# Performance work log

Measured on AMD Instinct MI355X. Metric: run time of the kernel, lower is better.

Reference implementation:

```python
import jax, jax.numpy as jnp
import numpy as np

N_NODES = 50000
N_EDGES = 800000
D_IN = 128
D_HID = 128
N_CLS = 40


def setup_inputs() -> dict:
    key = jax.random.key(0)
    ks = jax.random.split(key, 8)
    x = jax.random.normal(ks[0], (N_NODES, D_IN), dtype=jnp.float32)
    edge_index = jax.random.randint(ks[1], (2, N_EDGES), 0, N_NODES, dtype=jnp.int32)
    s1 = 1.0 / np.sqrt(D_IN)
    s2 = 1.0 / np.sqrt(D_HID)
    W1 = jax.random.normal(ks[2], (D_IN, D_HID), dtype=jnp.float32) * s1
    b1 = jnp.zeros((D_HID,), dtype=jnp.float32)
    W2 = jax.random.normal(ks[3], (D_HID, D_HID), dtype=jnp.float32) * s2
    b2 = jnp.zeros((D_HID,), dtype=jnp.float32)
    Wc = jax.random.normal(ks[4], (D_HID, N_CLS), dtype=jnp.float32) * s2
    bc = jnp.zeros((N_CLS,), dtype=jnp.float32)
    return {"x": x, "edge_index": edge_index, "W1": W1, "b1": b1,
            "W2": W2, "b2": b2, "Wc": Wc, "bc": bc, "conv_time": 30}


def _gcn_graph(edge_index, n, dtype):
    # add self-loops, compute symmetric GCN normalization D^-1/2 A D^-1/2
    loops = jnp.arange(n, dtype=edge_index.dtype)
    src = jnp.concatenate([edge_index[0], loops])
    dst = jnp.concatenate([edge_index[1], loops])
    deg = jax.ops.segment_sum(jnp.ones_like(src, dtype=dtype), dst, num_segments=n)
    dinv = jnp.where(deg > 0, jax.lax.rsqrt(jnp.maximum(deg, 1.0)), 0.0).astype(dtype)
    w = dinv[src] * dinv[dst]  # [E+N] edge weights
    return src, dst, w


def _propagate_k(h, src, dst, w, n, k):
    # apply normalized aggregation k times (k is a static Python int-compatible value)
    def body(_, hh):
        return jax.ops.segment_sum(hh[src] * w[:, None], dst, num_segments=n)
    return jax.lax.fori_loop(0, k, body, h)


def reference(x, edge_index, W1, b1, W2, b2, Wc, bc, conv_time):
    n = x.shape[0]
    src, dst, w = _gcn_graph(edge_index, n, x.dtype)
    # conv1: linear only (conv_time=0), relu; dropout is identity in eval mode
    h = jax.nn.relu(x @ W1 + b1)
    # conv2: linear + conv_time propagation hops, relu
    h = jax.nn.relu(_propagate_k(h @ W2 + b2, src, dst, w, n, conv_time))
    # cls: linear + 1 propagation hop
    out = _propagate_k(h @ Wc + bc, src, dst, w, n, 1)
    return out
```

## Files before the change

kernel.cpp:

```cpp
#include <hip/hip_runtime.h>
#include <hip/hip_bf16.h>

#define NN 50000
#define NE 800000
#define DH 128
#define NCLS 40
#define HOPS 30

typedef unsigned int uint32;
typedef unsigned short ushort16;


__global__ void count_deg(const int* __restrict__ dst, int* __restrict__ cnt) {
    int e = blockIdx.x * blockDim.x + threadIdx.x;
    if (e < NE) atomicAdd(&cnt[dst[e]], 1);
}

__global__ void calc_dinv(const int* __restrict__ cnt, float* __restrict__ dinv) {
    int v = blockIdx.x * blockDim.x + threadIdx.x;
    if (v < NN) dinv[v] = rsqrtf((float)cnt[v] + 1.0f);
}

__global__ void scan1(const int* __restrict__ cnt, int* __restrict__ rowptr,
                      int* __restrict__ bsum) {
    __shared__ int s[1024];
    int t = threadIdx.x;
    int i = blockIdx.x * 1024 + t;
    int v = (i < NN) ? cnt[i] : 0;
    s[t] = v;
    __syncthreads();
    for (int off = 1; off < 1024; off <<= 1) {
        int add = (t >= off) ? s[t - off] : 0;
        __syncthreads();
        s[t] += add;
        __syncthreads();
    }
    if (i < NN) rowptr[i] = s[t] - v;
    if (t == 1023) bsum[blockIdx.x] = s[1023];
}

__global__ void scan2(int* __restrict__ bsum, int* __restrict__ rowptr, int nb) {
    if (blockIdx.x == 0 && threadIdx.x == 0) {
        int run = 0;
        for (int b = 0; b < nb; ++b) { int v = bsum[b]; bsum[b] = run; run += v; }
        rowptr[NN] = run;
    }
}

__global__ void scan3(int* __restrict__ rowptr, const int* __restrict__ bsum,
                      int* __restrict__ cursor) {
    int i = blockIdx.x * 1024 + threadIdx.x;
    if (i < NN) {
        int r = rowptr[i] + bsum[blockIdx.x];
        rowptr[i] = r;
        cursor[i] = r;
    }
}

__global__ void fill_csr(const int* __restrict__ src, const int* __restrict__ dst,
                         const float* __restrict__ dinv, int* __restrict__ cursor,
                         int2* __restrict__ csr) {
    int e = blockIdx.x * blockDim.x + threadIdx.x;
    if (e < NE) {
        int s = src[e], d = dst[e];
        int p = atomicAdd(&cursor[d], 1);
        float w = dinv[s] * dinv[d];
        csr[p] = make_int2(s, __float_as_int(w));
    }
}


__device__ __forceinline__ void unpack8(uint4 u, float* f) {
    f[0] = __uint_as_float(u.x << 16);
    f[1] = __uint_as_float(u.x & 0xffff0000u);
    f[2] = __uint_as_float(u.y << 16);
    f[3] = __uint_as_float(u.y & 0xffff0000u);
    f[4] = __uint_as_float(u.z << 16);
    f[5] = __uint_as_float(u.z & 0xffff0000u);
    f[6] = __uint_as_float(u.w << 16);
    f[7] = __uint_as_float(u.w & 0xffff0000u);
}

__device__ __forceinline__ ushort16 f2bf(float x) {
    __hip_bfloat16 b = __float2bfloat16(x);
    return *reinterpret_cast<ushort16*>(&b);
}


template <bool RELU, bool BF16OUT>
__global__ __launch_bounds__(256) void gemm128(const float* __restrict__ A,
                                               const float* __restrict__ W,
                                               const float* __restrict__ bias,
                                               void* __restrict__ C, int n) {
    __shared__ float xs[64 * 128];
    __shared__ float ws[32 * 128];
    const int t = threadIdx.x;
    const int row0 = blockIdx.x * 64;

    const float4* A4 = reinterpret_cast<const float4*>(A);
    float4* xs4 = reinterpret_cast<float4*>(xs);
    for (int i = t; i < 64 * 32; i += 256) {
        int r = i >> 5, c4 = i & 31;
        int gr = row0 + r;
        xs4[i] = (gr < n) ? A4[(size_t)gr * 32 + c4] : make_float4(0.f, 0.f, 0.f, 0.f);
    }

    float acc[8][4];
#pragma unroll
    for (int r = 0; r < 8; ++r)
#pragma unroll
        for (int j = 0; j < 4; ++j) acc[r][j] = 0.f;

    const int cb = (t & 31) * 4;
    const int rb = (t >> 5) * 8;
    const float4* W4 = reinterpret_cast<const float4*>(W);
    float4* ws4 = reinterpret_cast<float4*>(ws);

    for (int k0 = 0; k0 < 128; k0 += 32) {
        __syncthreads();
        for (int i = t; i < 32 * 32; i += 256)
            ws4[i] = W4[(size_t)(k0 + (i >> 5)) * 32 + (i & 31)];
        __syncthreads();
#pragma unroll
        for (int kk = 0; kk < 32; ++kk) {
            float4 wv = ws4[kk * 32 + (cb >> 2)];
#pragma unroll
            for (int r = 0; r < 8; ++r) {
                float xv = xs[(rb + r) * 128 + k0 + kk];
                acc[r][0] += xv * wv.x;
                acc[r][1] += xv * wv.y;
                acc[r][2] += xv * wv.z;
                acc[r][3] += xv * wv.w;
            }
        }
    }

    float4 bv = reinterpret_cast<const float4*>(bias)[cb >> 2];
#pragma unroll
    for (int r = 0; r < 8; ++r) {
        int gr = row0 + rb + r;
        if (gr < n) {
            float o[4];
            o[0] = acc[r][0] + bv.x;
            o[1] = acc[r][1] + bv.y;
            o[2] = acc[r][2] + bv.z;
            o[3] = acc[r][3] + bv.w;
            if (RELU) {
#pragma unroll
                for (int j = 0; j < 4; ++j) o[j] = fmaxf(o[j], 0.f);
            }
            if (BF16OUT) {
                ushort16 pk[4];
#pragma unroll
                for (int j = 0; j < 4; ++j) pk[j] = f2bf(o[j]);
                *reinterpret_cast<ushort4*>(reinterpret_cast<ushort16*>(C) +
                                            (size_t)gr * 128 + cb) =
                    *reinterpret_cast<ushort4*>(pk);
            } else {
                float4 ov = make_float4(o[0], o[1], o[2], o[3]);
                reinterpret_cast<float4*>(C)[(size_t)gr * 32 + (cb >> 2)] = ov;
            }
        }
    }
}

__global__ __launch_bounds__(256) void gemm40_bf(const uint4* __restrict__ A,
                                                 const float* __restrict__ W,
                                                 const float* __restrict__ bias,
                                                 float* __restrict__ C, int n) {
    __shared__ float xs[32 * 128];
    __shared__ float wl[128 * 40];
    __shared__ float bl[40];
    const int t = threadIdx.x;
    const int row0 = blockIdx.x * 32;

    for (int i = t; i < 32 * 16; i += 256) {
        int r = i >> 4, c = i & 15, gr = row0 + r;
        uint4 u = (gr < n) ? A[(size_t)gr * 16 + c] : make_uint4(0, 0, 0, 0);
        float f[8];
        unpack8(u, f);
#pragma unroll
        for (int j = 0; j < 8; ++j) xs[r * 128 + c * 8 + j] = f[j];
    }
    for (int i = t; i < 128 * 40; i += 256) wl[i] = W[i];
    if (t < 40) bl[t] = bias[t];
    __syncthreads();

    const int r = t >> 3;
    const int c0 = (t & 7) * 5;
    float acc[5] = {0.f, 0.f, 0.f, 0.f, 0.f};
    for (int k = 0; k < 128; ++k) {
        float xv = xs[r * 128 + k];
#pragma unroll
        for (int j = 0; j < 5; ++j) acc[j] += xv * wl[k * 40 + c0 + j];
    }
    int gr = row0 + r;
    if (gr < n) {
#pragma unroll
        for (int j = 0; j < 5; ++j) C[(size_t)gr * 40 + c0 + j] = acc[j] + bl[c0 + j];
    }
}


__global__ __launch_bounds__(256) void prop_bf(const uint4* __restrict__ hin,
                                               uint4* __restrict__ hout,
                                               const int* __restrict__ rowptr,
                                               const int2* __restrict__ csr,
                                               const float* __restrict__ dinv,
                                               int relu) {
    const int g = threadIdx.x >> 4;
    const int l = threadIdx.x & 15;
    const int v = blockIdx.x * 16 + g;
    if (v >= NN) return;

    const float dv = dinv[v];
    const float wself = dv * dv;

    float acc[8];
    {
        float f[8];
        unpack8(hin[(size_t)v * 16 + l], f);
#pragma unroll
        for (int j = 0; j < 8; ++j) acc[j] = wself * f[j];
    }

    int e = rowptr[v];
    const int end = rowptr[v + 1];
    for (; e + 2 <= end; e += 2) {
        int2 p0 = csr[e];
        int2 p1 = csr[e + 1];
        uint4 a = hin[(size_t)p0.x * 16 + l];
        uint4 b = hin[(size_t)p1.x * 16 + l];
        float w0 = __int_as_float(p0.y);
        float w1 = __int_as_float(p1.y);
        float fa[8], fb[8];
        unpack8(a, fa);
        unpack8(b, fb);
#pragma unroll
        for (int j = 0; j < 8; ++j) acc[j] += w0 * fa[j] + w1 * fb[j];
    }
    if (e < end) {
        int2 p0 = csr[e];
        uint4 a = hin[(size_t)p0.x * 16 + l];
        float w0 = __int_as_float(p0.y);
        float fa[8];
        unpack8(a, fa);
#pragma unroll
        for (int j = 0; j < 8; ++j) acc[j] += w0 * fa[j];
    }

    if (relu) {
#pragma unroll
        for (int j = 0; j < 8; ++j) acc[j] = fmaxf(acc[j], 0.f);
    }

    ushort16 pk[8];
#pragma unroll
    for (int j = 0; j < 8; ++j) pk[j] = f2bf(acc[j]);
    hout[(size_t)v * 16 + l] = *reinterpret_cast<uint4*>(pk);
}

__global__ __launch_bounds__(64) void prop40(const float* __restrict__ z,
                                             float* __restrict__ out,
                                             const int* __restrict__ rowptr,
                                             const int2* __restrict__ csr,
                                             const float* __restrict__ dinv) {
    const int v = blockIdx.x;
    const int d = threadIdx.x;
    if (d >= NCLS) return;
    float dv = dinv[v];
    float acc = dv * dv * z[(size_t)v * NCLS + d];
    const int beg = rowptr[v], end = rowptr[v + 1];
    for (int e = beg; e < end; ++e) {
        int2 p = csr[e];
        acc += __int_as_float(p.y) * z[(size_t)p.x * NCLS + d];
    }
    out[(size_t)v * NCLS + d] = acc;
}


extern "C" void kernel_launch(void* const* d_in, const int* in_sizes, int n_in,
                              void* d_out, int out_size, void* d_ws, size_t ws_size,
                              hipStream_t stream) {
    const float* x   = (const float*)d_in[0];
    const int* edge  = (const int*)d_in[1];
    const float* W1  = (const float*)d_in[2];
    const float* b1  = (const float*)d_in[3];
    const float* W2  = (const float*)d_in[4];
    const float* b2  = (const float*)d_in[5];
    const float* Wc  = (const float*)d_in[6];
    const float* bc  = (const float*)d_in[7];
    const int* esrc = edge;
    const int* edst = edge + NE;
    float* out = (float*)d_out;

    char* w = (char*)d_ws;
    auto alloc = [&](size_t bytes) { void* p = (void*)w; w += (bytes + 255) & ~(size_t)255; return p; };
    int*   cnt    = (int*)  alloc((size_t)NN * 4);
    float* dinv   = (float*)alloc((size_t)NN * 4);
    int*   rowptr = (int*)  alloc((size_t)(NN + 1) * 4);
    int*   bsum   = (int*)  alloc(64 * 4);
    int*   cursor = (int*)  alloc((size_t)NN * 4);
    int2*  csr    = (int2*) alloc((size_t)NE * 8);
    float* h0f    = (float*)alloc((size_t)NN * DH * 4);
    uint4* hb0    = (uint4*)alloc((size_t)NN * DH * 2);
    uint4* hb1    = (uint4*)alloc((size_t)NN * DH * 2);
    float* z      = (float*)alloc((size_t)NN * NCLS * 4);

    const int NB_SCAN = (NN + 1023) / 1024;

    hipMemsetAsync(cnt, 0, (size_t)NN * 4, stream);
    count_deg<<<(NE + 255) / 256, 256, 0, stream>>>(edst, cnt);
    calc_dinv<<<(NN + 255) / 256, 256, 0, stream>>>(cnt, dinv);
    scan1<<<NB_SCAN, 1024, 0, stream>>>(cnt, rowptr, bsum);
    scan2<<<1, 64, 0, stream>>>(bsum, rowptr, NB_SCAN);
    scan3<<<NB_SCAN, 1024, 0, stream>>>(rowptr, bsum, cursor);
    fill_csr<<<(NE + 255) / 256, 256, 0, stream>>>(esrc, edst, dinv, cursor, csr);

    gemm128<true, false><<<(NN + 63) / 64, 256, 0, stream>>>(x, W1, b1, h0f, NN);
    gemm128<false, true><<<(NN + 63) / 64, 256, 0, stream>>>(h0f, W2, b2, hb0, NN);

    uint4* cur = hb0;
    uint4* alt = hb1;
    for (int hop = 0; hop < HOPS; ++hop) {
        prop_bf<<<(NN + 15) / 16, 256, 0, stream>>>(cur, alt, rowptr, csr, dinv,
                                                    (hop == HOPS - 1) ? 1 : 0);
        uint4* tmp = cur; cur = alt; alt = tmp;
    }

    gemm40_bf<<<(NN + 31) / 32, 256, 0, stream>>>(cur, Wc, bc, z, NN);
    prop40<<<NN, 64, 0, stream>>>(z, out, rowptr, csr, dinv);
}
```

Measured before the change: 1.274 ms.

## Use MFMA bf16 GEMMs, feature-sliced propagation, and reorder final propagate before classifier

Replaces the FP32 SIMT GEMMs with bf16 MFMA kernels using pre-transposed bf16 weights. Propagation now splits the 128 features into 8 column slices, one per block, so each hop works on a narrower cache footprint. It also stores only source indices in the CSR and computes edge weights from dinv on the fly. The last hop runs on the 128-wide hidden state before the classifier GEMM (A(hW)=(Ah)W), with the bias scaled by per-node row sums, which removes the narrow prop40 kernel. The input x is now rounded to bf16 before the first GEMM, which reduces precision.

```diff
diff --git a/kernel.cpp b/kernel.cpp
--- a/kernel.cpp
+++ b/kernel.cpp
@@ -9,6 +9,29 @@
 
 typedef unsigned int uint32;
 typedef unsigned short ushort16;
+typedef __attribute__((ext_vector_type(8))) short short8v;
+typedef __attribute__((ext_vector_type(4))) float float4v;
+
+
+__device__ __forceinline__ ushort16 bfbits(float x) {
+    __hip_bfloat16 b = __float2bfloat16(x);
+    return *reinterpret_cast<ushort16*>(&b);
+}
+
+__device__ __forceinline__ void unpack8(uint4 u, float* f) {
+    f[0] = __uint_as_float(u.x << 16);
+    f[1] = __uint_as_float(u.x & 0xffff0000u);
+    f[2] = __uint_as_float(u.y << 16);
+    f[3] = __uint_as_float(u.y & 0xffff0000u);
+    f[4] = __uint_as_float(u.z << 16);
+    f[5] = __uint_as_float(u.z & 0xffff0000u);
+    f[6] = __uint_as_float(u.w << 16);
+    f[7] = __uint_as_float(u.w & 0xffff0000u);
+}
+
+__device__ __forceinline__ uint32 pack2(float a, float b) {
+    return (uint32)bfbits(a) | ((uint32)bfbits(b) << 16);
+}
 
 
 __global__ void count_deg(const int* __restrict__ dst, int* __restrict__ cnt) {
@@ -58,132 +81,207 @@
 }
 
 __global__ void fill_csr(const int* __restrict__ src, const int* __restrict__ dst,
-                         const float* __restrict__ dinv, int* __restrict__ cursor,
-                         int2* __restrict__ csr) {
+                         int* __restrict__ cursor, int* __restrict__ csr_src) {
     int e = blockIdx.x * blockDim.x + threadIdx.x;
     if (e < NE) {
         int s = src[e], d = dst[e];
         int p = atomicAdd(&cursor[d], 1);
-        float w = dinv[s] * dinv[d];
-        csr[p] = make_int2(s, __float_as_int(w));
-    }
-}
-
-
-__device__ __forceinline__ void unpack8(uint4 u, float* f) {
-    f[0] = __uint_as_float(u.x << 16);
-    f[1] = __uint_as_float(u.x & 0xffff0000u);
-    f[2] = __uint_as_float(u.y << 16);
-    f[3] = __uint_as_float(u.y & 0xffff0000u);
-    f[4] = __uint_as_float(u.z << 16);
-    f[5] = __uint_as_float(u.z & 0xffff0000u);
-    f[6] = __uint_as_float(u.w << 16);
-    f[7] = __uint_as_float(u.w & 0xffff0000u);
-}
-
-__device__ __forceinline__ ushort16 f2bf(float x) {
-    __hip_bfloat16 b = __float2bfloat16(x);
-    return *reinterpret_cast<ushort16*>(&b);
-}
-
-
-template <bool RELU, bool BF16OUT>
-__global__ __launch_bounds__(256) void gemm128(const float* __restrict__ A,
-                                               const float* __restrict__ W,
-                                               const float* __restrict__ bias,
-                                               void* __restrict__ C, int n) {
-    __shared__ float xs[64 * 128];
-    __shared__ float ws[32 * 128];
+        csr_src[p] = s;
+    }
+}
+
+
+__global__ void prep_wt(const float* __restrict__ W1, const float* __restrict__ W2,
+                        ushort16* __restrict__ w1t, ushort16* __restrict__ w2t) {
+    int i = blockIdx.x * 256 + threadIdx.x;
+    if (i < 16384) {
+        int n = i >> 7, k = i & 127;
+        w1t[n * 128 + k] = bfbits(W1[k * 128 + n]);
+    } else {
+        int j = i - 16384;
+        int n = j >> 7, k = j & 127;
+        w2t[n * 128 + k] = bfbits(W2[k * 128 + n]);
+    }
+}
+
+
+template <bool AF32, bool RELU>
+__global__ __launch_bounds__(256) void conv_mfma(const void* __restrict__ Ap,
+                                                 const ushort16* __restrict__ WT,
+                                                 const float* __restrict__ bias,
+                                                 ushort16* __restrict__ C) {
     const int t = threadIdx.x;
-    const int row0 = blockIdx.x * 64;
-
-    const float4* A4 = reinterpret_cast<const float4*>(A);
-    float4* xs4 = reinterpret_cast<float4*>(xs);
-    for (int i = t; i < 64 * 32; i += 256) {
-        int r = i >> 5, c4 = i & 31;
-        int gr = row0 + r;
-        xs4[i] = (gr < n) ? A4[(size_t)gr * 32 + c4] : make_float4(0.f, 0.f, 0.f, 0.f);
-    }
-
-    float acc[8][4];
-#pragma unroll
-    for (int r = 0; r < 8; ++r)
-#pragma unroll
-        for (int j = 0; j < 4; ++j) acc[r][j] = 0.f;
-
-    const int cb = (t & 31) * 4;
-    const int rb = (t >> 5) * 8;
-    const float4* W4 = reinterpret_cast<const float4*>(W);
-    float4* ws4 = reinterpret_cast<float4*>(ws);
-
-    for (int k0 = 0; k0 < 128; k0 += 32) {
-        __syncthreads();
-        for (int i = t; i < 32 * 32; i += 256)
-            ws4[i] = W4[(size_t)(k0 + (i >> 5)) * 32 + (i & 31)];
-        __syncthreads();
-#pragma unroll
-        for (int kk = 0; kk < 32; ++kk) {
-            float4 wv = ws4[kk * 32 + (cb >> 2)];
-#pragma unroll
-            for (int r = 0; r < 8; ++r) {
-                float xv = xs[(rb + r) * 128 + k0 + kk];
-                acc[r][0] += xv * wv.x;
-                acc[r][1] += xv * wv.y;
-                acc[r][2] += xv * wv.z;
-                acc[r][3] += xv * wv.w;
+    const int w = t >> 6;
+    const int l = t & 63;
+    const int rb = blockIdx.x * 128 + w * 32;
+    const int lr = l & 15;
+    const int lk = (l >> 4) * 8;
+
+    short8v afr[2][4];
+#pragma unroll
+    for (int rt = 0; rt < 2; ++rt) {
+        int row = rb + rt * 16 + lr;
+        if (row > NN - 1) row = NN - 1;
+#pragma unroll
+        for (int ks = 0; ks < 4; ++ks) {
+            int k0 = ks * 32 + lk;
+            if (AF32) {
+                const float* ap = (const float*)Ap + (size_t)row * 128 + k0;
+                float4 f0 = *(const float4*)ap;
+                float4 f1 = *(const float4*)(ap + 4);
+                short8v s;
+                s[0] = (short)bfbits(f0.x); s[1] = (short)bfbits(f0.y);
+                s[2] = (short)bfbits(f0.z); s[3] = (short)bfbits(f0.w);
+                s[4] = (short)bfbits(f1.x); s[5] = (short)bfbits(f1.y);
+                s[6] = (short)bfbits(f1.z); s[7] = (short)bfbits(f1.w);
+                afr[rt][ks] = s;
+            } else {
+                afr[rt][ks] = *(const short8v*)((const ushort16*)Ap +
+                                                (size_t)row * 128 + k0);
             }
         }
     }
 
-    float4 bv = reinterpret_cast<const float4*>(bias)[cb >> 2];
-#pragma unroll
-    for (int r = 0; r < 8; ++r) {
-        int gr = row0 + rb + r;
-        if (gr < n) {
-            float o[4];
-            o[0] = acc[r][0] + bv.x;
-            o[1] = acc[r][1] + bv.y;
-            o[2] = acc[r][2] + bv.z;
-            o[3] = acc[r][3] + bv.w;
-            if (RELU) {
-#pragma unroll
-                for (int j = 0; j < 4; ++j) o[j] = fmaxf(o[j], 0.f);
-            }
-            if (BF16OUT) {
-                ushort16 pk[4];
-#pragma unroll
-                for (int j = 0; j < 4; ++j) pk[j] = f2bf(o[j]);
-                *reinterpret_cast<ushort4*>(reinterpret_cast<ushort16*>(C) +
-                                            (size_t)gr * 128 + cb) =
-                    *reinterpret_cast<ushort4*>(pk);
-            } else {
-                float4 ov = make_float4(o[0], o[1], o[2], o[3]);
-                reinterpret_cast<float4*>(C)[(size_t)gr * 32 + (cb >> 2)] = ov;
+    float4v acc[2][8];
+#pragma unroll
+    for (int rt = 0; rt < 2; ++rt)
+#pragma unroll
+        for (int ct = 0; ct < 8; ++ct)
+            acc[rt][ct] = (float4v){0.f, 0.f, 0.f, 0.f};
+
+#pragma unroll
+    for (int ks = 0; ks < 4; ++ks) {
+        short8v bfr[8];
+#pragma unroll
+        for (int ct = 0; ct < 8; ++ct)
+            bfr[ct] = *(const short8v*)(WT + (size_t)(ct * 16 + lr) * 128 +
+                                        ks * 32 + lk);
+#pragma unroll
+        for (int ct = 0; ct < 8; ++ct) {
+            acc[0][ct] = __builtin_amdgcn_mfma_f32_16x16x32_bf16(
+                afr[0][ks], bfr[ct], acc[0][ct], 0, 0, 0);
+            acc[1][ct] = __builtin_amdgcn_mfma_f32_16x16x32_bf16(
+                afr[1][ks], bfr[ct], acc[1][ct], 0, 0, 0);
+        }
+    }
+
+#pragma unroll
+    for (int ct = 0; ct < 8; ++ct) {
+        int col = ct * 16 + lr;
+        float bv = bias[col];
+#pragma unroll
+        for (int rt = 0; rt < 2; ++rt) {
+#pragma unroll
+            for (int r = 0; r < 4; ++r) {
+                int row = rb + rt * 16 + (l >> 4) * 4 + r;
+                if (row < NN) {
+                    float o = acc[rt][ct][r] + bv;
+                    if (RELU) o = fmaxf(o, 0.f);
+                    C[(size_t)row * 128 + col] = bfbits(o);
+                }
             }
         }
     }
 }
 
-__global__ __launch_bounds__(256) void gemm40_bf(const uint4* __restrict__ A,
-                                                 const float* __restrict__ W,
-                                                 const float* __restrict__ bias,
-                                                 float* __restrict__ C, int n) {
+
+__global__ __launch_bounds__(256) void prop_slice(const uint4* __restrict__ hin,
+                                                  void* __restrict__ hout,
+                                                  const int* __restrict__ rowptr,
+                                                  const int* __restrict__ csr_src,
+                                                  const float* __restrict__ dinv,
+                                                  float* __restrict__ psum,
+                                                  int relu, int last) {
+    const int s = blockIdx.x & 7;
+    const int p = blockIdx.x >> 3;
+    const int g = threadIdx.x >> 1;
+    const int l = threadIdx.x & 1;
+    const int v = p * 128 + g;
+    if (v >= NN) return;
+
+    const float dv = dinv[v];
+    const uint4* hb = hin + s * 2 + l;
+
+    float acc[8];
+    {
+        float f[8];
+        unpack8(hb[(size_t)v * 16], f);
+        const float ws = dv * dv;
+#pragma unroll
+        for (int j = 0; j < 8; ++j) acc[j] = ws * f[j];
+    }
+    float accp = dv * dv;
+
+    int e = rowptr[v];
+    const int end = rowptr[v + 1];
+    for (; e + 2 <= end; e += 2) {
+        int s0 = csr_src[e];
+        int s1 = csr_src[e + 1];
+        uint4 u0 = hb[(size_t)s0 * 16];
+        uint4 u1 = hb[(size_t)s1 * 16];
+        float w0 = dinv[s0] * dv;
+        float w1 = dinv[s1] * dv;
+        accp += w0 + w1;
+        float fa[8], fb[8];
+        unpack8(u0, fa);
+        unpack8(u1, fb);
+#pragma unroll
+        for (int j = 0; j < 8; ++j) acc[j] += w0 * fa[j] + w1 * fb[j];
+    }
+    if (e < end) {
+        int s0 = csr_src[e];
+        uint4 u0 = hb[(size_t)s0 * 16];
+        float w0 = dinv[s0] * dv;
+        accp += w0;
+        float fa[8];
+        unpack8(u0, fa);
+#pragma unroll
+        for (int j = 0; j < 8; ++j) acc[j] += w0 * fa[j];
+    }
+
+    if (relu) {
+#pragma unroll
+        for (int j = 0; j < 8; ++j) acc[j] = fmaxf(acc[j], 0.f);
+    }
+
+    if (!last) {
+        uint4 u;
+        u.x = pack2(acc[0], acc[1]);
+        u.y = pack2(acc[2], acc[3]);
+        u.z = pack2(acc[4], acc[5]);
+        u.w = pack2(acc[6], acc[7]);
+        ((uint4*)hout)[(size_t)v * 16 + s * 2 + l] = u;
+    } else {
+        float* qp = (float*)hout + (size_t)v * 128 + s * 16 + l * 8;
+        *(float4*)qp = make_float4(acc[0], acc[1], acc[2], acc[3]);
+        *(float4*)(qp + 4) = make_float4(acc[4], acc[5], acc[6], acc[7]);
+        if (s == 0 && l == 0) psum[v] = accp;
+    }
+}
+
+
+__global__ __launch_bounds__(256) void gemm40_psum(const float* __restrict__ A,
+                                                   const float* __restrict__ W,
+                                                   const float* __restrict__ bias,
+                                                   const float* __restrict__ psum,
+                                                   float* __restrict__ C) {
     __shared__ float xs[32 * 128];
     __shared__ float wl[128 * 40];
     __shared__ float bl[40];
+    __shared__ float ps[32];
     const int t = threadIdx.x;
     const int row0 = blockIdx.x * 32;
 
-    for (int i = t; i < 32 * 16; i += 256) {
-        int r = i >> 4, c = i & 15, gr = row0 + r;
-        uint4 u = (gr < n) ? A[(size_t)gr * 16 + c] : make_uint4(0, 0, 0, 0);
-        float f[8];
-        unpack8(u, f);
-#pragma unroll
-        for (int j = 0; j < 8; ++j) xs[r * 128 + c * 8 + j] = f[j];
+    const float4* A4 = reinterpret_cast<const float4*>(A);
+    float4* xs4 = reinterpret_cast<float4*>(xs);
+    for (int i = t; i < 32 * 32; i += 256) {
+        int r = i >> 5, gr = row0 + r;
+        xs4[i] = (gr < NN) ? A4[(size_t)gr * 32 + (i & 31)]
+                           : make_float4(0.f, 0.f, 0.f, 0.f);
     }
     for (int i = t; i < 128 * 40; i += 256) wl[i] = W[i];
     if (t < 40) bl[t] = bias[t];
+    if (t < 32) ps[t] = (row0 + t < NN) ? psum[row0 + t] : 0.f;
     __syncthreads();
 
     const int r = t >> 3;
@@ -195,87 +293,12 @@
         for (int j = 0; j < 5; ++j) acc[j] += xv * wl[k * 40 + c0 + j];
     }
     int gr = row0 + r;
-    if (gr < n) {
-#pragma unroll
-        for (int j = 0; j < 5; ++j) C[(size_t)gr * 40 + c0 + j] = acc[j] + bl[c0 + j];
-    }
-}
-
-
-__global__ __launch_bounds__(256) void prop_bf(const uint4* __restrict__ hin,
-                                               uint4* __restrict__ hout,
-                                               const int* __restrict__ rowptr,
-                                               const int2* __restrict__ csr,
-                                               const float* __restrict__ dinv,
-                                               int relu) {
-    const int g = threadIdx.x >> 4;
-    const int l = threadIdx.x & 15;
-    const int v = blockIdx.x * 16 + g;
-    if (v >= NN) return;
-
-    const float dv = dinv[v];
-    const float wself = dv * dv;
-
-    float acc[8];
-    {
-        float f[8];
-        unpack8(hin[(size_t)v * 16 + l], f);
-#pragma unroll
-        for (int j = 0; j < 8; ++j) acc[j] = wself * f[j];
-    }
-
-    int e = rowptr[v];
-    const int end = rowptr[v + 1];
-    for (; e + 2 <= end; e += 2) {
-        int2 p0 = csr[e];
-        int2 p1 = csr[e + 1];
-        uint4 a = hin[(size_t)p0.x * 16 + l];
-        uint4 b = hin[(size_t)p1.x * 16 + l];
-        float w0 = __int_as_float(p0.y);
-        float w1 = __int_as_float(p1.y);
-        float fa[8], fb[8];
-        unpack8(a, fa);
-        unpack8(b, fb);
-#pragma unroll
-        for (int j = 0; j < 8; ++j) acc[j] += w0 * fa[j] + w1 * fb[j];
-    }
-    if (e < end) {
-        int2 p0 = csr[e];
-        uint4 a = hin[(size_t)p0.x * 16 + l];
-        float w0 = __int_as_float(p0.y);
-        float fa[8];
-        unpack8(a, fa);
-#pragma unroll
-        for (int j = 0; j < 8; ++j) acc[j] += w0 * fa[j];
-    }
-
-    if (relu) {
-#pragma unroll
-        for (int j = 0; j < 8; ++j) acc[j] = fmaxf(acc[j], 0.f);
-    }
-
-    ushort16 pk[8];
-#pragma unroll
-    for (int j = 0; j < 8; ++j) pk[j] = f2bf(acc[j]);
-    hout[(size_t)v * 16 + l] = *reinterpret_cast<uint4*>(pk);
-}
-
-__global__ __launch_bounds__(64) void prop40(const float* __restrict__ z,
-                                             float* __restrict__ out,
-                                             const int* __restrict__ rowptr,
-                                             const int2* __restrict__ csr,
-                                             const float* __restrict__ dinv) {
-    const int v = blockIdx.x;
-    const int d = threadIdx.x;
-    if (d >= NCLS) return;
-    float dv = dinv[v];
-    float acc = dv * dv * z[(size_t)v * NCLS + d];
-    const int beg = rowptr[v], end = rowptr[v + 1];
-    for (int e = beg; e < end; ++e) {
-        int2 p = csr[e];
-        acc += __int_as_float(p.y) * z[(size_t)p.x * NCLS + d];
-    }
-    out[(size_t)v * NCLS + d] = acc;
+    if (gr < NN) {
+        float pv = ps[r];
+#pragma unroll
+        for (int j = 0; j < 5; ++j)
+            C[(size_t)gr * 40 + c0 + j] = acc[j] + pv * bl[c0 + j];
+    }
 }
 
 
@@ -296,18 +319,23 @@
 
     char* w = (char*)d_ws;
     auto alloc = [&](size_t bytes) { void* p = (void*)w; w += (bytes + 255) & ~(size_t)255; return p; };
-    int*   cnt    = (int*)  alloc((size_t)NN * 4);
-    float* dinv   = (float*)alloc((size_t)NN * 4);
-    int*   rowptr = (int*)  alloc((size_t)(NN + 1) * 4);
-    int*   bsum   = (int*)  alloc(64 * 4);
-    int*   cursor = (int*)  alloc((size_t)NN * 4);
-    int2*  csr    = (int2*) alloc((size_t)NE * 8);
-    float* h0f    = (float*)alloc((size_t)NN * DH * 4);
-    uint4* hb0    = (uint4*)alloc((size_t)NN * DH * 2);
-    uint4* hb1    = (uint4*)alloc((size_t)NN * DH * 2);
-    float* z      = (float*)alloc((size_t)NN * NCLS * 4);
+    int*      cnt     = (int*)     alloc((size_t)NN * 4);
+    float*    dinv    = (float*)   alloc((size_t)NN * 4);
+    int*      rowptr  = (int*)     alloc((size_t)(NN + 1) * 4);
+    int*      bsum    = (int*)     alloc(64 * 4);
+    int*      cursor  = (int*)     alloc((size_t)NN * 4);
+    int*      csr_src = (int*)     alloc((size_t)NE * 4);
+    ushort16* w1t     = (ushort16*)alloc(128 * 128 * 2);
+    ushort16* w2t     = (ushort16*)alloc(128 * 128 * 2);
+    ushort16* h0b     = (ushort16*)alloc((size_t)NN * DH * 2);
+    uint4*    hb0     = (uint4*)   alloc((size_t)NN * DH * 2);
+    uint4*    hb1     = (uint4*)   alloc((size_t)NN * DH * 2);
+    float*    q       = (float*)   alloc((size_t)NN * DH * 4);
+    float*    psum    = (float*)   alloc((size_t)NN * 4);
 
     const int NB_SCAN = (NN + 1023) / 1024;
+    const int NCHUNK = (NN + 127) / 128;
+    const int PROP_GRID = NCHUNK * 8;
 
     hipMemsetAsync(cnt, 0, (size_t)NN * 4, stream);
     count_deg<<<(NE + 255) / 256, 256, 0, stream>>>(edst, cnt);
@@ -315,19 +343,22 @@
     scan1<<<NB_SCAN, 1024, 0, stream>>>(cnt, rowptr, bsum);
     scan2<<<1, 64, 0, stream>>>(bsum, rowptr, NB_SCAN);
     scan3<<<NB_SCAN, 1024, 0, stream>>>(rowptr, bsum, cursor);
-    fill_csr<<<(NE + 255) / 256, 256, 0, stream>>>(esrc, edst, dinv, cursor, csr);
-
-    gemm128<true, false><<<(NN + 63) / 64, 256, 0, stream>>>(x, W1, b1, h0f, NN);
-    gemm128<false, true><<<(NN + 63) / 64, 256, 0, stream>>>(h0f, W2, b2, hb0, NN);
+    fill_csr<<<(NE + 255) / 256, 256, 0, stream>>>(esrc, edst, cursor, csr_src);
+    prep_wt<<<128, 256, 0, stream>>>(W1, W2, w1t, w2t);
+
+    conv_mfma<true, true><<<NCHUNK, 256, 0, stream>>>(x, w1t, b1, h0b);
+    conv_mfma<false, false><<<NCHUNK, 256, 0, stream>>>(h0b, w2t, b2,
+                                                        (ushort16*)hb0);
 
     uint4* cur = hb0;
     uint4* alt = hb1;
     for (int hop = 0; hop < HOPS; ++hop) {
-        prop_bf<<<(NN + 15) / 16, 256, 0, stream>>>(cur, alt, rowptr, csr, dinv,
-                                                    (hop == HOPS - 1) ? 1 : 0);
+        prop_slice<<<PROP_GRID, 256, 0, stream>>>(cur, alt, rowptr, csr_src, dinv,
+                                                  psum, (hop == HOPS - 1) ? 1 : 0, 0);
         uint4* tmp = cur; cur = alt; alt = tmp;
     }
-
-    gemm40_bf<<<(NN + 31) / 32, 256, 0, stream>>>(cur, Wc, bc, z, NN);
-    prop40<<<NN, 64, 0, stream>>>(z, out, rowptr, csr, dinv);
-}
+    prop_slice<<<PROP_GRID, 256, 0, stream>>>(cur, q, rowptr, csr_src, dinv,
+                                              psum, 0, 1);
+
+    gemm40_psum<<<(NN + 31) / 32, 256, 0, stream>>>(q, Wc, bc, psum, out);
+}
```

Measured after the change: 3.314 ms. +160.2%, slower.
